# Optimization experiments

Hardware: AMD Instinct MI355X
Metric: run time of the kernel (lower is better)

Reference implementation:

```python
import jax, jax.numpy as jnp
import numpy as np
import math

N_NODES = 4096
NUM_FEATURES = 500
NHID = 256
RATIO = 0.75


def _build_adj(x):
    # Faithful vectorization of get_threshold/get_edge_index:
    # t = 0.5 * max_{i,j} ||x_i - x_j||^2 ; directed edges (src=i -> dst=j) for j>i with d2<t.
    # Dense adjacency A[dst, src] (jit-friendly; edge count is data-dependent in the original).
    sq = jnp.sum(x * x, axis=1)
    d2 = sq[:, None] + sq[None, :] - 2.0 * (x @ x.T)  # [N,N] squared distances
    t = 0.5 * jnp.max(d2)
    N = x.shape[0]
    lower = jnp.tril(jnp.ones((N, N), dtype=bool), k=-1)  # entry [j,i], j>i
    return jnp.where(lower & (d2 < t), 1.0, 0.0).astype(x.dtype)


def _gcn(A, x, W, b):
    # PyG GCNConv: add self-loops, symmetric normalization D^-1/2 (A+I) D^-1/2, then @ (xW) + b
    N = A.shape[0]
    Ah = A + jnp.eye(N, dtype=A.dtype)
    dis = jax.lax.rsqrt(jnp.sum(Ah, axis=1))  # deg >= 1 due to self loops
    norm = (dis[:, None] * Ah) * dis[None, :]
    return norm @ (x @ W) + b


def _sag_pool(A, x, Wr, Wn, bn, k):
    # SAGPooling with default GraphConv scorer: score = sum-aggr(neighbors)@Wn + bn + x@Wr
    score = jnp.tanh(((A @ x) @ Wn + bn + x @ Wr)[:, 0])  # [N]
    vals, perm = jax.lax.top_k(score, k)  # top ceil(ratio*N) nodes, descending
    xp = x[perm] * vals[:, None]
    Ap = A[perm][:, perm]  # filter edges to surviving nodes
    return Ap, xp


def _readout(x):
    # single graph (batch=None -> all zeros): [gmp, gap] -> [1, 2*nhid]
    return jnp.concatenate([jnp.max(x, axis=0), jnp.mean(x, axis=0)])[None, :]


def setup_inputs() -> dict:
    key = jax.random.key(0)
    ks = jax.random.split(key, 16)
    s = 0.02
    inp = {
        "feature": jax.random.normal(ks[0], (N_NODES, NUM_FEATURES), jnp.float32),
        "img_info": jax.random.normal(ks[1], (N_NODES, 6), jnp.float32),
        "W_pos": jax.random.normal(ks[2], (6, 12), jnp.float32) * s,
        "b_pos": jnp.zeros((12,), jnp.float32),
        "W1": jax.random.normal(ks[3], (512, NHID), jnp.float32) * s,
        "b1": jnp.zeros((NHID,), jnp.float32),
        "W2": jax.random.normal(ks[4], (NHID, NHID), jnp.float32) * s,
        "b2": jnp.zeros((NHID,), jnp.float32),
        "W3": jax.random.normal(ks[5], (NHID, NHID), jnp.float32) * s,
        "b3": jnp.zeros((NHID,), jnp.float32),
        "Wr1": jax.random.normal(ks[6], (NHID, 1), jnp.float32) * s,
        "Wn1": jax.random.normal(ks[7], (NHID, 1), jnp.float32) * s,
        "bs1": jnp.zeros((1,), jnp.float32),
        "Wr2": jax.random.normal(ks[8], (NHID, 1), jnp.float32) * s,
        "Wn2": jax.random.normal(ks[9], (NHID, 1), jnp.float32) * s,
        "bs2": jnp.zeros((1,), jnp.float32),
        "Wr3": jax.random.normal(ks[10], (NHID, 1), jnp.float32) * s,
        "Wn3": jax.random.normal(ks[11], (NHID, 1), jnp.float32) * s,
        "bs3": jnp.zeros((1,), jnp.float32),
    }
    return inp


def reference(feature, img_info, W_pos, b_pos, W1, b1, W2, b2, W3, b3,
              Wr1, Wn1, bs1, Wr2, Wn2, bs2, Wr3, Wn3, bs3):
    pos = jax.nn.relu(img_info @ W_pos + b_pos)          # [N,12]
    feat = jnp.concatenate([feature, pos], axis=1)       # [N,512]
    N = feat.shape[0]
    k1 = math.ceil(RATIO * N)
    k2 = math.ceil(RATIO * k1)
    k3 = math.ceil(RATIO * k2)

    A = _build_adj(feat)

    x = jax.nn.relu(_gcn(A, feat, W1, b1))
    A, x = _sag_pool(A, x, Wr1, Wn1, bs1, k1)
    x1 = _readout(x)

    x = jax.nn.relu(_gcn(A, x, W2, b2))
    A, x = _sag_pool(A, x, Wr2, Wn2, bs2, k2)
    x2 = _readout(x)

    x = jax.nn.relu(_gcn(A, x, W3, b3))
    A, x = _sag_pool(A, x, Wr3, Wn3, bs3, k3)
    x3 = _readout(x)

    return x1 + x2 + x3  # [1, 2*NHID]
```

## Files before the change

kernel.cpp:

```cpp
#include <hip/hip_runtime.h>
#include <hip/hip_bf16.h>
#include <math.h>

typedef __hip_bfloat16 bf16;
typedef unsigned short ushort;
typedef unsigned int uint;
typedef unsigned long long ull;
static __device__ __forceinline__ float b2f(bf16 x){ return __bfloat162float(x); }

static __device__ __forceinline__ float ldf(const void* p, int i, int isbf){
    return isbf ? b2f(((const bf16*)p)[i]) : ((const float*)p)[i];
}
static __device__ __forceinline__ ushort f2b(float x){
    return __bfloat16_as_ushort(__float2bfloat16(x));
}
static __device__ __forceinline__ uint fcode(float v){
    uint u = __float_as_uint(v);
    return (u & 0x80000000u) ? ~u : (u | 0x80000000u);
}
static __device__ __forceinline__ float fdecode(uint c){
    uint u = (c & 0x80000000u) ? (c & 0x7FFFFFFFu) : ~c;
    return __uint_as_float(u);
}

#define NN    4096
#define FEAT0 500
#define DIN   512
#define NH    256
#define KL1   3072
#define KL2   2304
#define KL3   1728
#define EDGE_CAP 786432u

typedef __attribute__((ext_vector_type(8)))  short v8s;
typedef __attribute__((ext_vector_type(16))) float v16f;

static __device__ __forceinline__ void detect_bf16(const void* p, int n, int t,
        uint* flag){
    if (t < 256 && t < n){
        uint e = ((uint)((const ushort*)p)[t] >> 7) & 0xFFu;
        if (e >= 135u) atomicAnd(flag, 0u);
    }
}

struct DtIn { const void* p[19]; int n[19]; };
__global__ __launch_bounds__(512) void k_prep(DtIn da,
        ushort* __restrict__ Xb, float* __restrict__ sq, ushort* __restrict__ Wb,
        unsigned* __restrict__ dflag, float* __restrict__ degA,
        uint* __restrict__ maxU, float* __restrict__ sums,
        unsigned* __restrict__ ecnt, unsigned* __restrict__ maxd2,
        float* __restrict__ tmin){
    int row = blockIdx.x, t = threadIdx.x;
    if (row < NN){
        __shared__ uint fl[4];
        if (t < 4) fl[t] = 1u;
        __syncthreads();
        detect_bf16(da.p[0], da.n[0], t, &fl[0]);
        detect_bf16(da.p[1], da.n[1], t, &fl[1]);
        detect_bf16(da.p[2], da.n[2], t, &fl[2]);
        detect_bf16(da.p[3], da.n[3], t, &fl[3]);
        __syncthreads();
        int f_feat = (int)fl[0], f_img = (int)fl[1], f_wp = (int)fl[2], f_bp = (int)fl[3];
        float v;
        if (t < FEAT0) v = ldf(da.p[0], row*FEAT0 + t, f_feat);
        else {
            int c = t - FEAT0;
            float acc = ldf(da.p[3], c, f_bp);
            #pragma unroll
            for (int d = 0; d < 6; d++)
                acc += ldf(da.p[1], row*6+d, f_img) * ldf(da.p[2], d*12+c, f_wp);
            v = fmaxf(acc, 0.f);
        }
        bf16 vb = __float2bfloat16(v);
        Xb[row*DIN + t] = __bfloat16_as_ushort(vb);
        float vr = b2f(vb);
        __shared__ float red[512];
        red[t] = vr*vr;
        __syncthreads();
        for (int s = 256; s > 0; s >>= 1){ if (t < s) red[t] += red[t+s]; __syncthreads(); }
        if (t == 0) sq[row] = red[0];
    } else if (row < NN + 64){
        __shared__ uint fl[3];
        if (t < 3) fl[t] = 1u;
        __syncthreads();
        detect_bf16(da.p[4], da.n[4], t, &fl[0]);
        detect_bf16(da.p[6], da.n[6], t, &fl[1]);
        detect_bf16(da.p[8], da.n[8], t, &fl[2]);
        __syncthreads();
        int i0 = ((row - NN)*512 + t)*8;
        #pragma unroll
        for (int j = 0; j < 8; j++){
            int idx = i0 + j;
            float v;
            if (idx < 131072)       v = ldf(da.p[4], idx,          (int)fl[0]);
            else if (idx < 196608)  v = ldf(da.p[6], idx - 131072, (int)fl[1]);
            else                    v = ldf(da.p[8], idx - 196608, (int)fl[2]);
            Wb[idx] = __bfloat16_as_ushort(__float2bfloat16(v));
        }
    } else {
        for (int i = t; i < NN; i += 512) degA[i] = 1.0f;
        for (int i = t; i < 4096; i += 512) tmin[i] = INFINITY;
        for (int i = t; i < 768; i += 512){ maxU[i] = 0x007FFFFFu; sums[i] = 0.f; }
        if (t == 0){ ecnt[0]=0u; ecnt[1]=0u; ecnt[2]=0u; ecnt[3]=0u; maxd2[0]=0u; }
        if (t < 19){
            const unsigned short* h = (const unsigned short*)da.p[t];
            int n = da.n[t]; if (n > 256) n = 256;
            int isbf = 1;
            for (int j = 0; j < n; j++){
                uint e = ((uint)h[j] >> 7) & 0xFFu;
                if (e >= 135u) isbf = 0;
            }
            dflag[t] = (unsigned)isbf;
        }
    }
}

static __device__ __forceinline__ v16f mm_tile(const ushort* __restrict__ Arows,
        const ushort* __restrict__ Brows, int K, ushort* As, ushort* Bs,
        int tid, int wv, int l31, int hi){
    int row0 = tid >> 3, g0 = tid & 7;
    int row1 = row0 + 32;
    int d0 = row0*64 + ((g0^(row0&7))<<3);
    int d1 = row1*64 + ((g0^(row1&7))<<3);
    int wwr = wv >> 1, wwc = wv & 1;
    int ra0 = (wwr*32 + l31)*64, rbp = (wwc*32 + l31)*64;
    int fr7a = (wwr*32 + l31) & 7, fr7b = (wwc*32 + l31) & 7;
    float4 a0p = *(const float4*)(Arows + (size_t)row0*K + g0*8);
    float4 a1p = *(const float4*)(Arows + (size_t)row1*K + g0*8);
    float4 b0p = *(const float4*)(Brows + (size_t)row0*K + g0*8);
    float4 b1p = *(const float4*)(Brows + (size_t)row1*K + g0*8);
    v16f acc = {};
    int NC = K >> 6;
    for (int c = 0; c < NC; c++){
        __syncthreads();
        *(float4*)&As[d0] = a0p; *(float4*)&As[d1] = a1p;
        *(float4*)&Bs[d0] = b0p; *(float4*)&Bs[d1] = b1p;
        __syncthreads();
        if (c + 1 < NC){
            int k0 = (c+1)*64;
            a0p = *(const float4*)(Arows + (size_t)row0*K + k0 + g0*8);
            a1p = *(const float4*)(Arows + (size_t)row1*K + k0 + g0*8);
            b0p = *(const float4*)(Brows + (size_t)row0*K + k0 + g0*8);
            b1p = *(const float4*)(Brows + (size_t)row1*K + k0 + g0*8);
        }
        #pragma unroll
        for (int ks = 0; ks < 4; ks++){
            int gq = ks*2 + hi;
            v8s a = *(const v8s*)&As[ra0 + ((gq^fr7a)<<3)];
            v8s b = *(const v8s*)&Bs[rbp + ((gq^fr7b)<<3)];
            acc = __builtin_amdgcn_mfma_f32_32x32x16_bf16(a, b, acc, 0, 0, 0);
        }
    }
    return acc;
}

static __device__ __forceinline__ void xw_body(const ushort* __restrict__ Ab,
        const ushort* __restrict__ Wb, float* __restrict__ XW, int rb, int cb,
        int K, ushort* As, ushort* Bs){
    int tid = threadIdx.x, lane = tid & 63, wv = tid >> 6;
    int wwr = wv >> 1, wwc = wv & 1;
    int l31 = lane & 31, hi = lane >> 5;
    int arow0 = tid >> 3, ag = tid & 7;
    int arow1 = arow0 + 32;
    int da0 = arow0*64 + ((ag^(arow0&7))<<3);
    int da1 = arow1*64 + ((ag^(arow1&7))<<3);
    const size_t baseA = (size_t)rb*64*K;
    int kr = tid >> 2, ng = tid & 3;
    float4 a0p = *(const float4*)(Ab + baseA + (size_t)arow0*K + ag*8);
    float4 a1p = *(const float4*)(Ab + baseA + (size_t)arow1*K + ag*8);
    float4 b0p = *(const float4*)(Wb + (size_t)kr*NH + cb*64 + ng*16);
    float4 b1p = *(const float4*)(Wb + (size_t)kr*NH + cb*64 + ng*16 + 8);
    v16f acc = {};
    int ra0 = (wwr*32 + l31)*64, rbp = (wwc*32 + l31)*64;
    int fr7a = (wwr*32 + l31) & 7, fr7b = (wwc*32 + l31) & 7;
    int kg = kr >> 3, k7 = kr & 7;
    int NC = K >> 6;
    for (int c = 0; c < NC; c++){
        __syncthreads();
        *(float4*)&As[da0] = a0p; *(float4*)&As[da1] = a1p;
        const ushort* bw0 = (const ushort*)&b0p;
        const ushort* bw1 = (const ushort*)&b1p;
        #pragma unroll
        for (int j = 0; j < 8; j++){
            int nn = ng*16 + j;
            Bs[nn*64 + ((kg^(nn&7))<<3) + k7] = bw0[j];
        }
        #pragma unroll
        for (int j = 0; j < 8; j++){
            int nn = ng*16 + 8 + j;
            Bs[nn*64 + ((kg^(nn&7))<<3) + k7] = bw1[j];
        }
        __syncthreads();
        if (c + 1 < NC){
            int k0 = (c+1)*64;
            a0p = *(const float4*)(Ab + baseA + (size_t)arow0*K + k0 + ag*8);
            a1p = *(const float4*)(Ab + baseA + (size_t)arow1*K + k0 + ag*8);
            b0p = *(const float4*)(Wb + (size_t)(k0+kr)*NH + cb*64 + ng*16);
            b1p = *(const float4*)(Wb + (size_t)(k0+kr)*NH + cb*64 + ng*16 + 8);
        }
        #pragma unroll
        for (int ks = 0; ks < 4; ks++){
            int gq = ks*2 + hi;
            v8s a = *(const v8s*)&As[ra0 + ((gq^fr7a)<<3)];
            v8s b = *(const v8s*)&Bs[rbp + ((gq^fr7b)<<3)];
            acc = __builtin_amdgcn_mfma_f32_32x32x16_bf16(a, b, acc, 0, 0, 0);
        }
    }
    int n  = cb*64 + wwc*32 + l31;
    int mb = rb*64 + wwr*32 + 4*hi;
    #pragma unroll
    for (int i = 0; i < 16; i++){
        int m = mb + (i&3) + 8*(i>>2);
        XW[(size_t)m*NH + n] = acc[i];
    }
}

template<int PASS>
__global__ __launch_bounds__(256) void k_gram(const ushort* __restrict__ Xb,
        const float* __restrict__ sq, unsigned* __restrict__ maxd2,
        float* __restrict__ tmin, unsigned* __restrict__ ecnt,
        unsigned* __restrict__ edges, float* __restrict__ deg,
        const ushort* __restrict__ Wb, float* __restrict__ XW){
    __shared__ __align__(16) ushort As[64*64];
    __shared__ __align__(16) ushort Bs[64*64];
    int rb = blockIdx.x, cb = blockIdx.y;
    if (PASS == 1 && cb >= 64){
        xw_body(Xb, Wb, XW, rb, cb - 64, DIN, As, Bs);
        return;
    }
    if (cb > rb) return;
    int tid = threadIdx.x;
    float tthr = 0.f;
    if (PASS == 2){
        tthr = 0.5f * __uint_as_float(maxd2[0]);
        if (tmin[rb*64 + cb] >= tthr) return;
    }
    int lane = tid & 63, wv = tid >> 6;
    int l31 = lane & 31, hi = lane >> 5;
    int wwr = wv >> 1, wwc = wv & 1;
    v16f acc = mm_tile(Xb + (size_t)rb*64*DIN, Xb + (size_t)cb*64*DIN, DIN,
                       As, Bs, tid, wv, l31, hi);
    int rbase = rb*64 + wwr*32 + 4*hi;
    int col   = cb*64 + wwc*32 + l31;
    float sqc = sq[col];
    if (PASS == 1){
        float m = 0.f, mn = INFINITY;
        #pragma unroll
        for (int i = 0; i < 16; i++){
            int r = rbase + (i&3) + 8*(i>>2);
            float d2 = sq[r] + sqc - 2.f*acc[i];
            if (r != col) m = fmaxf(m, d2);
            if (r > col)  mn = fminf(mn, d2);
        }
        #pragma unroll
        for (int off = 32; off >= 1; off >>= 1){
            m  = fmaxf(m,  __shfl_down(m,  off));
            mn = fminf(mn, __shfl_down(mn, off));
        }
        __shared__ float wmax[4], wmin[4];
        if (lane == 0){ wmax[wv] = m; wmin[wv] = mn; }
        __syncthreads();
        if (tid == 0){
            float mm = fmaxf(fmaxf(wmax[0], wmax[1]), fmaxf(wmax[2], wmax[3]));
            tmin[rb*64 + cb] = fminf(fminf(wmin[0], wmin[1]), fminf(wmin[2], wmin[3]));
            atomicMax(maxd2, __float_as_uint(fmaxf(mm, 0.f)));
        }
    } else {
        #pragma unroll
        for (int i = 0; i < 16; i++){
            int r = rbase + (i&3) + 8*(i>>2);
            float d2 = sq[r] + sqc - 2.f*acc[i];
            if (r > col && d2 < tthr){
                unsigned idx = atomicAdd(ecnt, 1u);
                if (idx < EDGE_CAP){
                    edges[idx] = ((unsigned)r << 16) | (unsigned)col;
                    atomicAdd(&deg[r], 1.0f);
                }
            }
        }
    }
}

__global__ __launch_bounds__(256) void k_xwp(const float* __restrict__ Xn,
        const int* __restrict__ perm, const float* __restrict__ svals,
        const ushort* __restrict__ Wb, float* __restrict__ XW, int M,
        uint* __restrict__ maxU, float* __restrict__ sums, int layer){
    int rb = blockIdx.x, cb = blockIdx.y;
    __shared__ __align__(16) ushort As[64*64];
    __shared__ __align__(16) ushort Bs[64*64];
    __shared__ float pmx[256], psm[256];
    int tid = threadIdx.x, lane = tid & 63, wv = tid >> 6;
    int wwr = wv >> 1, wwc = wv & 1;
    int l31 = lane & 31, hi = lane >> 5;
    int arow0 = tid >> 3, ag = tid & 7;
    int arow1 = arow0 + 32;
    int da0 = arow0*64 + ((ag^(arow0&7))<<3);
    int da1 = arow1*64 + ((ag^(arow1&7))<<3);
    int p0 = perm[rb*64 + arow0]; float sv0 = svals[rb*64 + arow0];
    int p1 = perm[rb*64 + arow1]; float sv1 = svals[rb*64 + arow1];
    int kr = tid >> 2, ng = tid & 3;
    int kg = kr >> 3, k7 = kr & 7;
    int ra0 = (wwr*32 + l31)*64, rbp = (wwc*32 + l31)*64;
    int fr7a = (wwr*32 + l31) & 7, fr7b = (wwc*32 + l31) & 7;

    float4 xa0 = *(const float4*)(Xn + (size_t)p0*NH + ag*8);
    float4 xa1 = *(const float4*)(Xn + (size_t)p0*NH + ag*8 + 4);
    float4 xb0 = *(const float4*)(Xn + (size_t)p1*NH + ag*8);
    float4 xb1 = *(const float4*)(Xn + (size_t)p1*NH + ag*8 + 4);
    float4 wb0 = *(const float4*)(Wb + (size_t)kr*NH + cb*64 + ng*16);
    float4 wb1 = *(const float4*)(Wb + (size_t)kr*NH + cb*64 + ng*16 + 8);

    v16f acc = {};
    for (int c = 0; c < 4; c++){
        __syncthreads();
        {
            __align__(16) ushort ta[8];
            ta[0]=f2b(xa0.x*sv0); ta[1]=f2b(xa0.y*sv0); ta[2]=f2b(xa0.z*sv0); ta[3]=f2b(xa0.w*sv0);
            ta[4]=f2b(xa1.x*sv0); ta[5]=f2b(xa1.y*sv0); ta[6]=f2b(xa1.z*sv0); ta[7]=f2b(xa1.w*sv0);
            *(float4*)&As[da0] = *(const float4*)ta;
            __align__(16) ushort tb[8];
            tb[0]=f2b(xb0.x*sv1); tb[1]=f2b(xb0.y*sv1); tb[2]=f2b(xb0.z*sv1); tb[3]=f2b(xb0.w*sv1);
            tb[4]=f2b(xb1.x*sv1); tb[5]=f2b(xb1.y*sv1); tb[6]=f2b(xb1.z*sv1); tb[7]=f2b(xb1.w*sv1);
            *(float4*)&As[da1] = *(const float4*)tb;
        }
        {
            const ushort* bw0 = (const ushort*)&wb0;
            const ushort* bw1 = (const ushort*)&wb1;
            #pragma unroll
            for (int j = 0; j < 8; j++){
                int nn = ng*16 + j;
                Bs[nn*64 + ((kg^(nn&7))<<3) + k7] = bw0[j];
            }
            #pragma unroll
            for (int j = 0; j < 8; j++){
                int nn = ng*16 + 8 + j;
                Bs[nn*64 + ((kg^(nn&7))<<3) + k7] = bw1[j];
            }
        }
        __syncthreads();
        if (c < 3){
            int k0 = (c+1)*64;
            xa0 = *(const float4*)(Xn + (size_t)p0*NH + k0 + ag*8);
            xa1 = *(const float4*)(Xn + (size_t)p0*NH + k0 + ag*8 + 4);
            xb0 = *(const float4*)(Xn + (size_t)p1*NH + k0 + ag*8);
            xb1 = *(const float4*)(Xn + (size_t)p1*NH + k0 + ag*8 + 4);
            wb0 = *(const float4*)(Wb + (size_t)(k0+kr)*NH + cb*64 + ng*16);
            wb1 = *(const float4*)(Wb + (size_t)(k0+kr)*NH + cb*64 + ng*16 + 8);
        }
        if (cb == 0){
            int cc = tid & 63, q = tid >> 6;
            int gg = cc >> 3, c7 = cc & 7;
            float m = -INFINITY, s = 0.f;
            #pragma unroll
            for (int i = 0; i < 16; i++){
                int rr = q*16 + i;
                float v = __uint_as_float(((uint)As[rr*64 + ((gg^(rr&7))<<3) + c7]) << 16);
                m = fmaxf(m, v); s += v;
            }
            pmx[tid] = m; psm[tid] = s;
            __syncthreads();
            if (tid < 64){
                float mm = fmaxf(fmaxf(pmx[tid], pmx[tid+64]), fmaxf(pmx[tid+128], pmx[tid+192]));
                float ss = psm[tid] + psm[tid+64] + psm[tid+128] + psm[tid+192];
                atomicMax(&maxU[layer*NH + c*64 + tid], fcode(mm));
                atomicAdd(&sums[layer*NH + c*64 + tid], ss);
            }
        }
        #pragma unroll
        for (int ks = 0; ks < 4; ks++){
            int gq = ks*2 + hi;
            v8s a = *(const v8s*)&As[ra0 + ((gq^fr7a)<<3)];
            v8s b = *(const v8s*)&Bs[rbp + ((gq^fr7b)<<3)];
            acc = __builtin_amdgcn_mfma_f32_32x32x16_bf16(a, b, acc, 0, 0, 0);
        }
    }
    int n  = cb*64 + wwc*32 + l31;
    int mb = rb*64 + wwr*32 + 4*hi;
    #pragma unroll
    for (int i = 0; i < 16; i++){
        int m = mb + (i&3) + 8*(i>>2);
        XW[(size_t)m*NH + n] = acc[i];
    }
}

__global__ __launch_bounds__(256) void k_gcnscore(const float* __restrict__ XW,
        const unsigned* __restrict__ edges, const unsigned* __restrict__ ecnt, int slot,
        const float* __restrict__ deg, const void* __restrict__ b,
        const void* __restrict__ Wn, const void* __restrict__ Wr, const void* __restrict__ bs,
        const unsigned* __restrict__ fb, const unsigned* __restrict__ fWn,
        const unsigned* __restrict__ fWr, const unsigned* __restrict__ fbs,
        float* __restrict__ Xn, float* __restrict__ s1, float* __restrict__ z){
    int row = blockIdx.x, t = threadIdx.x;
    __shared__ unsigned eL[256];
    __shared__ unsigned Esh;
    if (t == 0){ unsigned E0 = ecnt[slot]; Esh = (E0 > EDGE_CAP) ? EDGE_CAP : E0; }
    __syncthreads();
    unsigned E = Esh;
    float disr = 1.0f / sqrtf(deg[row]);
    float acc = disr * XW[row*NH + t];
    for (unsigned base = 0; base < E; base += 256){
        unsigned nchunk = E - base; if (nchunk > 256) nchunk = 256;
        __syncthreads();
        if (t < nchunk) eL[t] = edges[base + t];
        __syncthreads();
        for (unsigned j = 0; j < nchunk; j++){
            unsigned ed = eL[j];
            if ((int)(ed >> 16) == row){
                int src = ed & 0xFFFFu;
                acc += (1.0f / sqrtf(deg[src])) * XW[src*NH + t];
            }
        }
    }
    float xn = fmaxf(fmaf(disr, acc, ldf(b, t, (int)fb[0])), 0.f);
    Xn[row*NH + t] = xn;
    float a  = xn * ldf(Wn, t, (int)fWn[0]);
    float bb = xn * ldf(Wr, t, (int)fWr[0]);
    for (int off = 32; off >= 1; off >>= 1){ a += __shfl_down(a, off); bb += __shfl_down(bb, off); }
    __shared__ float ra[4], rbv[4];
    int w = t >> 6;
    if ((t & 63) == 0){ ra[w] = a; rbv[w] = bb; }
    __syncthreads();
    if (t == 0){
        s1[row] = ra[0]+ra[1]+ra[2]+ra[3];
        z[row]  = rbv[0]+rbv[1]+rbv[2]+rbv[3] + ldf(bs, 0, (int)fbs[0]);
    }
}

static __device__ __forceinline__ uint2 radix_scan(const uint* hist, uint* wt,
        uint* ws, uint* sh, int t, int lane, int wv, uint kk, int NB){
    uint loc = 0;
    int b0 = t << 2;
    if (b0 < NB) loc = hist[b0] + hist[b0+1] + hist[b0+2] + hist[b0+3];
    uint s = loc;
    #pragma unroll
    for (int off = 1; off < 64; off <<= 1){
        uint u = __shfl_down(s, off);
        if (lane + off < 64) s += u;
    }
    if (lane == 0) wt[wv] = s;
    __syncthreads();
    if (t < 16){
        uint a = 0;
        for (int j = t + 1; j < 16; j++) a += wt[j];
        ws[t] = a;
    }
    __syncthreads();
    if (b0 < NB){
        uint run = ws[wv] + (s - loc);
        for (int b = b0 + 3; b >= b0; b--){
            uint h = hist[b];
            if (run < kk && run + h >= kk){ sh[0] = (uint)b; sh[1] = run; }
            run += h;
        }
    }
    __syncthreads();
    return make_uint2(sh[0], sh[1]);
}

__global__ __launch_bounds__(1024) void k_select(const float* __restrict__ z,
        const float* __restrict__ s1, int N, int k,
        const unsigned* __restrict__ eIn, unsigned* __restrict__ ecnt, int slotCur,
        unsigned* __restrict__ eOut, int slotOut,
        int* __restrict__ perm, float* __restrict__ svals,
        float* __restrict__ degN, int Nnext){
    __shared__ float zsh[4096];
    __shared__ int   rnk[4096];
    __shared__ uint  hist[4096];
    __shared__ uint  wcnt[16];
    __shared__ uint  wbase[16];
    __shared__ uint  sh[4];
    int t = threadIdx.x;
    int lane = t & 63, wv = t >> 6;
    for (int i = t; i < N; i += 1024){ zsh[i] = z[i]; rnk[i] = -1; }
    for (int i = t; i < Nnext; i += 1024) degN[i] = 1.0f;
    if (t == 0) sh[2] = 0u;
    __syncthreads();
    unsigned E = ecnt[slotCur]; if (E > EDGE_CAP) E = EDGE_CAP;
    for (unsigned e = t; e < E; e += 1024){
        unsigned ed = eIn[e];
        atomicAdd(&zsh[ed >> 16], s1[ed & 0xFFFFu]);
    }
    __syncthreads();
    bool v0 = t < N,        v1 = t+1024 < N,  v2 = t+2048 < N,  v3 = t+3072 < N;
    uint c0 = v0 ? fcode(zsh[t])      : 0u;
    uint c1 = v1 ? fcode(zsh[t+1024]) : 0u;
    uint c2 = v2 ? fcode(zsh[t+2048]) : 0u;
    uint c3 = v3 ? fcode(zsh[t+3072]) : 0u;

    for (int i = t; i < 4096; i += 1024) hist[i] = 0u;
    __syncthreads();
    if (v0) atomicAdd(&hist[c0 >> 20], 1u);
    if (v1) atomicAdd(&hist[c1 >> 20], 1u);
    if (v2) atomicAdd(&hist[c2 >> 20], 1u);
    if (v3) atomicAdd(&hist[c3 >> 20], 1u);
    __syncthreads();
    uint2 p1 = radix_scan(hist, wcnt, wbase, sh, t, lane, wv, (uint)k, 4096);
    uint B1 = p1.x; uint kk2 = (uint)k - p1.y;
    for (int i = t; i < 4096; i += 1024) hist[i] = 0u;
    __syncthreads();
    if (v0 && (c0 >> 20) == B1) atomicAdd(&hist[(c0 >> 8) & 0xFFFu], 1u);
    if (v1 && (c1 >> 20) == B1) atomicAdd(&hist[(c1 >> 8) & 0xFFFu], 1u);
    if (v2 && (c2 >> 20) == B1) atomicAdd(&hist[(c2 >> 8) & 0xFFFu], 1u);
    if (v3 && (c3 >> 20) == B1) atomicAdd(&hist[(c3 >> 8) & 0xFFFu], 1u);
    __syncthreads();
    uint2 p2 = radix_scan(hist, wcnt, wbase, sh, t, lane, wv, kk2, 4096);
    uint B2 = p2.x; uint kk3 = kk2 - p2.y;
    uint hi24 = (B1 << 12) | B2;
    for (int i = t; i < 256; i += 1024) hist[i] = 0u;
    __syncthreads();
    if (v0 && (c0 >> 8) == hi24) atomicAdd(&hist[c0 & 0xFFu], 1u);
    if (v1 && (c1 >> 8) == hi24) atomicAdd(&hist[c1 & 0xFFu], 1u);
    if (v2 && (c2 >> 8) == hi24) atomicAdd(&hist[c2 & 0xFFu], 1u);
    if (v3 && (c3 >> 8) == hi24) atomicAdd(&hist[c3 & 0xFFu], 1u);
    __syncthreads();
    uint2 p3 = radix_scan(hist, wcnt, wbase, sh, t, lane, wv, kk3, 256);
    uint T = (B1 << 20) | (B2 << 8) | p3.x;

    ull b0 = __ballot(v0 && c0 > T), b1 = __ballot(v1 && c1 > T);
    ull b2 = __ballot(v2 && c2 > T), b3 = __ballot(v3 && c3 > T);
    uint t0 = (uint)__popcll(b0), t1 = (uint)__popcll(b1);
    uint t2 = (uint)__popcll(b2), t3 = (uint)__popcll(b3);
    if (lane == 0) wcnt[wv] = t0 + t1 + t2 + t3;
    __syncthreads();
    if (t == 0){
        uint s = 0;
        for (int i = 0; i < 16; i++){ wbase[i] = s; s += wcnt[i]; }
        sh[1] = s;
    }
    __syncthreads();
    uint cntGT = sh[1];
    uint rem = (uint)k - cntGT;
    ull ltm = ((ull)1 << lane) - 1;
    uint off = wbase[wv];
    if (v0 && c0 > T){ uint r = off + (uint)__popcll(b0 & ltm); int i = t;
        perm[r] = i; svals[r] = tanhf(zsh[i]); rnk[i] = (int)r; }
    off += t0;
    if (v1 && c1 > T){ uint r = off + (uint)__popcll(b1 & ltm); int i = t+1024;
        perm[r] = i; svals[r] = tanhf(zsh[i]); rnk[i] = (int)r; }
    off += t1;
    if (v2 && c2 > T){ uint r = off + (uint)__popcll(b2 & ltm); int i = t+2048;
        perm[r] = i; svals[r] = tanhf(zsh[i]); rnk[i] = (int)r; }
    off += t2;
    if (v3 && c3 > T){ uint r = off + (uint)__popcll(b3 & ltm); int i = t+3072;
        perm[r] = i; svals[r] = tanhf(zsh[i]); rnk[i] = (int)r; }
    #pragma unroll
    for (int j = 0; j < 4; j++){
        int i = t + j*1024;
        bool vv = (j==0) ? v0 : (j==1) ? v1 : (j==2) ? v2 : v3;
        uint cc = (j==0) ? c0 : (j==1) ? c1 : (j==2) ? c2 : c3;
        if (vv && cc == T){
            uint e = atomicAdd(&sh[2], 1u);
            if (e < rem){
                uint r = cntGT + e;
                perm[r] = i; svals[r] = tanhf(zsh[i]); rnk[i] = (int)r;
            }
        }
    }
    __syncthreads();
    if (slotOut >= 0){
        for (unsigned e = t; e < E; e += 1024){
            unsigned ed = eIn[e];
            int nd = rnk[ed >> 16], ns = rnk[ed & 0xFFFFu];
            if (nd >= 0 && ns >= 0){
                unsigned idx = atomicAdd(&ecnt[slotOut], 1u);
                if (idx < EDGE_CAP){
                    eOut[idx] = ((unsigned)nd << 16) | (unsigned)ns;
                    atomicAdd(&degN[nd], 1.0f);
                }
            }
        }
    }
}

__global__ __launch_bounds__(256) void k_poolread3(const float* __restrict__ Xn,
        const int* __restrict__ perm, const float* __restrict__ svals, int k,
        uint* __restrict__ maxU, float* __restrict__ sums,
        unsigned* __restrict__ done, float* __restrict__ out){
    int b = blockIdx.x, t = threadIdx.x;
    float m = -INFINITY, s = 0.f;
    for (int r = b; r < k; r += 64){
        int p = perm[r];
        float v = Xn[p*NH + t] * svals[r];
        m = fmaxf(m, v); s += v;
    }
    atomicMax(&maxU[2*NH + t], fcode(m));
    atomicAdd(&sums[2*NH + t], s);
    __threadfence();
    __shared__ uint lastv;
    if (t == 0) lastv = atomicAdd(done, 1u);
    __syncthreads();
    if (lastv == 63u){
        uint m0 = atomicAdd(&maxU[t], 0u);
        uint m1 = atomicAdd(&maxU[NH + t], 0u);
        uint m2 = atomicAdd(&maxU[2*NH + t], 0u);
        float s0 = atomicAdd(&sums[t], 0.f);
        float s1v = atomicAdd(&sums[NH + t], 0.f);
        float s2 = atomicAdd(&sums[2*NH + t], 0.f);
        out[t] = fdecode(m0) + fdecode(m1) + fdecode(m2);
        out[NH + t] = s0*(1.0f/KL1) + s1v*(1.0f/KL2) + s2*(1.0f/KL3);
    }
}

extern "C" void kernel_launch(void* const* d_in, const int* in_sizes, int n_in,
                              void* d_out, int out_size, void* d_ws, size_t ws_size,
                              hipStream_t stream)
{
    const void* b1 = d_in[5];
    const void* b2 = d_in[7];
    const void* b3 = d_in[9];
    const void* Wr1 = d_in[10]; const void* Wn1 = d_in[11]; const void* bs1 = d_in[12];
    const void* Wr2 = d_in[13]; const void* Wn2 = d_in[14]; const void* bs2 = d_in[15];
    const void* Wr3 = d_in[16]; const void* Wn3 = d_in[17]; const void* bs3 = d_in[18];

    char* w = (char*)d_ws;
    auto alloc = [&](size_t bytes)->char*{ char* p = w; w += (bytes + 255) & ~(size_t)255; return p; };
    ushort*   Xb    = (ushort*)  alloc((size_t)NN*DIN*2);
    float*    Xn    = (float*)   alloc((size_t)NN*NH*4);
    float*    XW    = (float*)   alloc((size_t)NN*NH*4);
    ushort*   Wb    = (ushort*)  alloc((size_t)262144*2);
    unsigned* E0    = (unsigned*)alloc((size_t)EDGE_CAP*4);
    unsigned* E1    = (unsigned*)alloc((size_t)EDGE_CAP*4);
    float*    tmin  = (float*)   alloc(4096*4);
    float*    sq    = (float*)   alloc(NN*4);
    float*    degA  = (float*)   alloc(NN*4);
    float*    degB  = (float*)   alloc(NN*4);
    float*    s1    = (float*)   alloc(NN*4);
    float*    z     = (float*)   alloc(NN*4);
    int*      perm  = (int*)     alloc(NN*4);
    float*    svals = (float*)   alloc(NN*4);
    unsigned* ecnt  = (unsigned*)alloc(256);
    unsigned* maxd2 = (unsigned*)alloc(256);
    unsigned* dflag = (unsigned*)alloc(256);
    uint*     maxU  = (uint*)    alloc(768*4);
    float*    sums  = (float*)   alloc(768*4);
    (void)ws_size;

    DtIn da;
    for (int i = 0; i < 19; i++){ da.p[i] = d_in[i]; da.n[i] = in_sizes[i]; }

    k_prep<<<NN + 65, 512, 0, stream>>>(da, Xb, sq, Wb, dflag, degA, maxU, sums,
            ecnt, maxd2, tmin);
    k_gram<1><<<dim3(64,68), 256, 0, stream>>>(Xb, sq, maxd2, tmin, ecnt, E0, degA,
            Wb, XW);
    k_gram<2><<<dim3(64,64), 256, 0, stream>>>(Xb, sq, maxd2, tmin, ecnt, E0, degA,
            Wb, XW);

    k_gcnscore<<<NN, 256, 0, stream>>>(XW, E0, ecnt, 0, degA, b1, Wn1, Wr1, bs1,
            dflag+5, dflag+11, dflag+10, dflag+12, Xn, s1, z);
    k_select<<<1, 1024, 0, stream>>>(z, s1, NN, KL1, E0, ecnt, 0, E1, 1,
            perm, svals, degB, KL1);

    k_xwp<<<dim3(48,4), 256, 0, stream>>>(Xn, perm, svals, Wb + 131072, XW, KL1,
            maxU, sums, 0);
    k_gcnscore<<<KL1, 256, 0, stream>>>(XW, E1, ecnt, 1, degB, b2, Wn2, Wr2, bs2,
            dflag+7, dflag+14, dflag+13, dflag+15, Xn, s1, z);
    k_select<<<1, 1024, 0, stream>>>(z, s1, KL1, KL2, E1, ecnt, 1, E0, 2,
            perm, svals, degA, KL2);

    k_xwp<<<dim3(36,4), 256, 0, stream>>>(Xn, perm, svals, Wb + 196608, XW, KL2,
            maxU, sums, 1);
    k_gcnscore<<<KL2, 256, 0, stream>>>(XW, E0, ecnt, 2, degA, b3, Wn3, Wr3, bs3,
            dflag+9, dflag+17, dflag+16, dflag+18, Xn, s1, z);
    k_select<<<1, 1024, 0, stream>>>(z, s1, KL2, KL3, E0, ecnt, 2,
            (unsigned*)nullptr, -1, perm, svals, degB, 0);
    k_poolread3<<<64, 256, 0, stream>>>(Xn, perm, svals, KL3, maxU, sums,
            ecnt + 3, (float*)d_out);
}
```

Measured before the change: 236.8 us.

## Launch only lower-triangular gram tiles and fuse final readout into select

The gram kernels now launch a 1D grid covering only the lower-triangular 64x64 tile pairs, recovering (rb, cb) from the linear index, instead of a full 2D grid where the upper half exits immediately. The k_poolread3 kernel is removed and the last pooling readout plus output combination run inside the final single-block k_select. Separately, the row squared-norm reduction in prep switches from a shared-memory tree to wavefront shuffles. These changes cut launch count and the empty-block scheduling overhead, at the cost of doing the final readout on one 1024-thread block.

```diff
diff --git a/kernel.cpp b/kernel.cpp
--- a/kernel.cpp
+++ b/kernel.cpp
@@ -31,6 +31,7 @@
 #define KL2   2304
 #define KL3   1728
 #define EDGE_CAP 786432u
+#define NTRI  2080
 
 typedef __attribute__((ext_vector_type(8)))  short v8s;
 typedef __attribute__((ext_vector_type(16))) float v16f;
@@ -74,11 +75,18 @@
         bf16 vb = __float2bfloat16(v);
         Xb[row*DIN + t] = __bfloat16_as_ushort(vb);
         float vr = b2f(vb);
-        __shared__ float red[512];
-        red[t] = vr*vr;
-        __syncthreads();
-        for (int s = 256; s > 0; s >>= 1){ if (t < s) red[t] += red[t+s]; __syncthreads(); }
-        if (t == 0) sq[row] = red[0];
+        float vsq = vr*vr;
+        #pragma unroll
+        for (int off = 32; off >= 1; off >>= 1) vsq += __shfl_down(vsq, off);
+        __shared__ float red[8];
+        if ((t & 63) == 0) red[t >> 6] = vsq;
+        __syncthreads();
+        if (t == 0){
+            float sres = 0.f;
+            #pragma unroll
+            for (int i = 0; i < 8; i++) sres += red[i];
+            sq[row] = sres;
+        }
     } else if (row < NN + 64){
         __shared__ uint fl[3];
         if (t < 3) fl[t] = 1u;
@@ -101,7 +109,11 @@
         for (int i = t; i < NN; i += 512) degA[i] = 1.0f;
         for (int i = t; i < 4096; i += 512) tmin[i] = INFINITY;
         for (int i = t; i < 768; i += 512){ maxU[i] = 0x007FFFFFu; sums[i] = 0.f; }
-        if (t == 0){ ecnt[0]=0u; ecnt[1]=0u; ecnt[2]=0u; ecnt[3]=0u; maxd2[0]=0u; }
+        if (t == 0){
+            #pragma unroll
+            for (int i = 0; i < 8; i++) ecnt[i] = 0u;
+            maxd2[0] = 0u;
+        }
         if (t < 19){
             const unsigned short* h = (const unsigned short*)da.p[t];
             int n = da.n[t]; if (n > 256) n = 256;
@@ -223,12 +235,20 @@
         const ushort* __restrict__ Wb, float* __restrict__ XW){
     __shared__ __align__(16) ushort As[64*64];
     __shared__ __align__(16) ushort Bs[64*64];
-    int rb = blockIdx.x, cb = blockIdx.y;
-    if (PASS == 1 && cb >= 64){
-        xw_body(Xb, Wb, XW, rb, cb - 64, DIN, As, Bs);
-        return;
-    }
-    if (cb > rb) return;
+    int b = blockIdx.x;
+    if (PASS == 1){
+        if (b < 256){
+            xw_body(Xb, Wb, XW, b >> 2, b & 3, DIN, As, Bs);
+            return;
+        }
+        b -= 256;
+    }
+    float ff = sqrtf(8.f*(float)b + 1.f);
+    int rb = (int)((ff - 1.f) * 0.5f);
+    while ((rb+1)*(rb+2)/2 <= b) rb++;
+    while (rb*(rb+1)/2 > b) rb--;
+    int cb = b - rb*(rb+1)/2;
+
     int tid = threadIdx.x;
     float tthr = 0.f;
     if (PASS == 2){
@@ -462,7 +482,9 @@
         const unsigned* __restrict__ eIn, unsigned* __restrict__ ecnt, int slotCur,
         unsigned* __restrict__ eOut, int slotOut,
         int* __restrict__ perm, float* __restrict__ svals,
-        float* __restrict__ degN, int Nnext){
+        float* __restrict__ degN, int Nnext,
+        const float* __restrict__ Xn, const uint* __restrict__ maxU,
+        const float* __restrict__ sums, float* __restrict__ outp){
     __shared__ float zsh[4096];
     __shared__ int   rnk[4096];
     __shared__ uint  hist[4096];
@@ -569,35 +591,24 @@
                 }
             }
         }
-    }
-}
-
-__global__ __launch_bounds__(256) void k_poolread3(const float* __restrict__ Xn,
-        const int* __restrict__ perm, const float* __restrict__ svals, int k,
-        uint* __restrict__ maxU, float* __restrict__ sums,
-        unsigned* __restrict__ done, float* __restrict__ out){
-    int b = blockIdx.x, t = threadIdx.x;
-    float m = -INFINITY, s = 0.f;
-    for (int r = b; r < k; r += 64){
-        int p = perm[r];
-        float v = Xn[p*NH + t] * svals[r];
-        m = fmaxf(m, v); s += v;
-    }
-    atomicMax(&maxU[2*NH + t], fcode(m));
-    atomicAdd(&sums[2*NH + t], s);
-    __threadfence();
-    __shared__ uint lastv;
-    if (t == 0) lastv = atomicAdd(done, 1u);
-    __syncthreads();
-    if (lastv == 63u){
-        uint m0 = atomicAdd(&maxU[t], 0u);
-        uint m1 = atomicAdd(&maxU[NH + t], 0u);
-        uint m2 = atomicAdd(&maxU[2*NH + t], 0u);
-        float s0 = atomicAdd(&sums[t], 0.f);
-        float s1v = atomicAdd(&sums[NH + t], 0.f);
-        float s2 = atomicAdd(&sums[2*NH + t], 0.f);
-        out[t] = fdecode(m0) + fdecode(m1) + fdecode(m2);
-        out[NH + t] = s0*(1.0f/KL1) + s1v*(1.0f/KL2) + s2*(1.0f/KL3);
+    } else {
+        int col = t & 255, g = t >> 8;
+        float m = -INFINITY, s = 0.f;
+        for (int r = g; r < k; r += 4){
+            int p = perm[r];
+            float v = Xn[(size_t)p*NH + col] * svals[r];
+            m = fmaxf(m, v); s += v;
+        }
+        __syncthreads();
+        zsh[g*256 + col] = m;
+        zsh[1024 + g*256 + col] = s;
+        __syncthreads();
+        if (t < NH){
+            float mm = fmaxf(fmaxf(zsh[t], zsh[256+t]), fmaxf(zsh[512+t], zsh[768+t]));
+            float ss = zsh[1024+t] + zsh[1280+t] + zsh[1536+t] + zsh[1792+t];
+            outp[t]      = fdecode(maxU[t]) + fdecode(maxU[NH+t]) + mm;
+            outp[NH + t] = sums[t]*(1.0f/KL1) + sums[NH+t]*(1.0f/KL2) + ss*(1.0f/KL3);
+        }
     }
 }
 
@@ -640,29 +651,28 @@
 
     k_prep<<<NN + 65, 512, 0, stream>>>(da, Xb, sq, Wb, dflag, degA, maxU, sums,
             ecnt, maxd2, tmin);
-    k_gram<1><<<dim3(64,68), 256, 0, stream>>>(Xb, sq, maxd2, tmin, ecnt, E0, degA,
+    k_gram<1><<<256 + NTRI, 256, 0, stream>>>(Xb, sq, maxd2, tmin, ecnt, E0, degA,
             Wb, XW);
-    k_gram<2><<<dim3(64,64), 256, 0, stream>>>(Xb, sq, maxd2, tmin, ecnt, E0, degA,
+    k_gram<2><<<NTRI, 256, 0, stream>>>(Xb, sq, maxd2, tmin, ecnt, E0, degA,
             Wb, XW);
 
     k_gcnscore<<<NN, 256, 0, stream>>>(XW, E0, ecnt, 0, degA, b1, Wn1, Wr1, bs1,
             dflag+5, dflag+11, dflag+10, dflag+12, Xn, s1, z);
     k_select<<<1, 1024, 0, stream>>>(z, s1, NN, KL1, E0, ecnt, 0, E1, 1,
-            perm, svals, degB, KL1);
+            perm, svals, degB, KL1, Xn, maxU, sums, (float*)d_out);
 
     k_xwp<<<dim3(48,4), 256, 0, stream>>>(Xn, perm, svals, Wb + 131072, XW, KL1,
             maxU, sums, 0);
     k_gcnscore<<<KL1, 256, 0, stream>>>(XW, E1, ecnt, 1, degB, b2, Wn2, Wr2, bs2,
             dflag+7, dflag+14, dflag+13, dflag+15, Xn, s1, z);
     k_select<<<1, 1024, 0, stream>>>(z, s1, KL1, KL2, E1, ecnt, 1, E0, 2,
-            perm, svals, degA, KL2);
+            perm, svals, degA, KL2, Xn, maxU, sums, (float*)d_out);
 
     k_xwp<<<dim3(36,4), 256, 0, stream>>>(Xn, perm, svals, Wb + 196608, XW, KL2,
             maxU, sums, 1);
     k_gcnscore<<<KL2, 256, 0, stream>>>(XW, E0, ecnt, 2, degA, b3, Wn3, Wr3, bs3,
             dflag+9, dflag+17, dflag+16, dflag+18, Xn, s1, z);
     k_select<<<1, 1024, 0, stream>>>(z, s1, KL2, KL3, E0, ecnt, 2,
-            (unsigned*)nullptr, -1, perm, svals, degB, 0);
-    k_poolread3<<<64, 256, 0, stream>>>(Xn, perm, svals, KL3, maxU, sums,
-            ecnt + 3, (float*)d_out);
-}
+            (unsigned*)nullptr, -1, perm, svals, degB, 0,
+            Xn, maxU, sums, (float*)d_out);
+}
```

Result: slower. 445.7 us (+88.2%).
